# Optimization experiments

Hardware: AMD Instinct MI355X
Metric: run time of the kernel (lower is better)

The kernel has to match this reference:

```python
import jax, jax.numpy as jnp
import numpy as np
from jax import lax

B, IC, OC, H, W_DIM, K = 8, 64, 64, 256, 512, 3
BLUR_1D = [1.0, 3.0, 3.0, 1.0]
FACTOR = 2
GAIN = 1.0


def _blur_kernel():
    # setup_resample_kernel: outer product of 1D kernel, normalized to sum 1
    k = np.asarray(BLUR_1D, dtype=np.float32)
    k = np.outer(k, k)
    k = k / np.sum(k)
    return k  # [4,4]


def setup_inputs() -> dict:
    key = jax.random.key(0)
    ks = jax.random.split(key, 5)
    x = jax.random.normal(ks[0], (B, IC, H, H), dtype=jnp.float32)
    w = jax.random.normal(ks[1], (B, W_DIM), dtype=jnp.float32)
    # init_std = 1.0 for both weights since lrmul = 1.0
    w_conv = jax.random.normal(ks[2], (K, K, IC, OC), dtype=jnp.float32)
    w_dense = jax.random.normal(ks[3], (W_DIM, IC), dtype=jnp.float32)
    b_mod = jnp.zeros((IC,), dtype=jnp.float32)
    return {"x": x, "w": w, "w_conv": w_conv, "w_dense": w_dense, "b_mod": b_mod}


def reference(x, w, w_conv, w_dense, b_mod):
    k = w_conv.shape[0]
    ic, oc = w_conv.shape[2], w_conv.shape[3]

    # runtime coefs (equalized lr): he_std = gain / sqrt(fan_in), lrmul = 1
    coef_conv = 1.0 / np.sqrt(k * k * ic)
    coef_dense = 1.0 / np.sqrt(w.shape[1])

    # style = Dense(w) + bias (linear act, gain 1) + 1.0   -> [B, IC]
    style = w @ (coef_dense * w_dense) + b_mod + 1.0

    # modulate: [B,k,k,IC,OC]
    wmod = (coef_conv * w_conv)[None] * style[:, None, None, :, None]
    # demodulate over (kh, kw, ic)
    d = lax.rsqrt(jnp.sum(jnp.square(wmod), axis=(1, 2, 3)) + 1e-8)  # [B,OC]
    wmod = wmod * d[:, None, None, None, :]

    # per-sample grouped transposed conv (upsample x2) == lhs-dilated cross-corr
    # with the unflipped modulated weight, padding k-1 on each side.
    w_oihw = jnp.transpose(wmod, (0, 4, 3, 1, 2))  # [B,OC,IC,k,k]

    def up_conv(xb, wb):
        return lax.conv_general_dilated(
            xb[None], wb, window_strides=(1, 1),
            padding=[(k - 1, k - 1), (k - 1, k - 1)],
            lhs_dilation=(FACTOR, FACTOR),
            dimension_numbers=("NCHW", "OIHW", "NCHW"))[0]

    y = jax.vmap(up_conv)(x, w_oihw)  # [B,OC,(H-1)*2+k,(W-1)*2+k] = [B,OC,513,513]

    # upfirdn blur: kernel scaled by gain * factor**2, pad0 = pad1 = 1,
    # true convolution (kernel flipped in reference) applied depthwise.
    kb = jnp.asarray(_blur_kernel() * (GAIN * FACTOR ** 2))  # [4,4]
    fw = kb[::-1, ::-1][None, None]  # [1,1,4,4]
    b_, c_, s1, s2 = y.shape
    y = lax.conv_general_dilated(
        y.reshape(b_ * c_, 1, s1, s2), fw, window_strides=(1, 1),
        padding=[(1, 1), (1, 1)],
        dimension_numbers=("NCHW", "OIHW", "NCHW"))
    # output spatial: s1 + 2 - 4 + 1 = 2H
    return y.reshape(b_, c_, y.shape[2], y.shape[3])
```

## Files before the change

kernel.cpp:

```cpp
#include <hip/hip_runtime.h>

#define NB 8
#define IC 64
#define OC 64
#define HH 256
#define WD 512
#define PP 258

typedef __bf16 bf16x8 __attribute__((ext_vector_type(8)));
typedef float f32x16 __attribute__((ext_vector_type(16)));
typedef float f32x2 __attribute__((ext_vector_type(2)));

__device__ inline void compute_E(const float* __restrict__ w_conv, float stv,
                                 int oc, float E[6][6]) {
  const float coef_conv = 1.0f / 24.0f;
  const float s = stv * coef_conv;
  const int ic = threadIdx.x & 63;

  float wm[3][3];
  float ssq = 0.f;
  #pragma unroll
  for (int kh = 0; kh < 3; ++kh)
    #pragma unroll
    for (int kw = 0; kw < 3; ++kw) {
      float v = w_conv[((kh * 3 + kw) * IC + ic) * OC + oc] * s;
      wm[kh][kw] = v;
      ssq += v * v;
    }
  #pragma unroll
  for (int off = 32; off > 0; off >>= 1) ssq += __shfl_xor(ssq, off);
  const float d = rsqrtf(ssq + 1e-8f);
  #pragma unroll
  for (int kh = 0; kh < 3; ++kh)
    #pragma unroll
    for (int kw = 0; kw < 3; ++kw) wm[kh][kw] *= d;

  const float g[4] = {0.25f, 0.75f, 0.75f, 0.25f};
  #pragma unroll
  for (int a = 0; a < 6; ++a)
    #pragma unroll
    for (int c = 0; c < 6; ++c) {
      float acc = 0.f;
      #pragma unroll
      for (int dh = 0; dh < 3; ++dh) {
        int u = a - dh;
        if (u < 0 || u > 3) continue;
        #pragma unroll
        for (int dw = 0; dw < 3; ++dw) {
          int v = c - dw;
          if (v < 0 || v > 3) continue;
          acc = fmaf(wm[dh][dw], g[u] * g[v], acc);
        }
      }
      E[a][c] = acc;
    }
}

__device__ inline float style_of(const float* __restrict__ w,
                                 const float* __restrict__ w_dense,
                                 const float* __restrict__ b_mod, int b,
                                 int ic) {
  const float coef_dense = 0.044194173824159216f;
  const float* wr = w + b * WD;
  float acc = 0.f;
  for (int k = 0; k < WD; ++k) acc = fmaf(wr[k], w_dense[k * IC + ic], acc);
  return acc * coef_dense + b_mod[ic] + 1.0f;
}

__global__ __launch_bounds__(64) void pwfs_kernel(
    const float* __restrict__ w, const float* __restrict__ w_dense,
    const float* __restrict__ b_mod, const float* __restrict__ w_conv,
    __bf16* __restrict__ PWf) {
  const int oc = blockIdx.x;
  const int b = blockIdx.y;
  const int ic = threadIdx.x;

  float stv = style_of(w, w_dense, b_mod, b, ic);
  float E[6][6];
  compute_E(w_conv, stv, oc, E);

  const int ks = ic >> 4;
  const int h = (ic >> 3) & 1;
  const int e = ic & 7;
  const int lane = (oc & 31) + 32 * h;
  const int ocg = oc >> 5;

  #pragma unroll
  for (int pp = 0; pp < 2; ++pp)
    #pragma unroll
    for (int pq = 0; pq < 2; ++pq) {
      const int ph = pp * 2 + pq;
      #pragma unroll
      for (int j = 0; j < 3; ++j)
        #pragma unroll
        for (int l = 0; l < 3; ++l) {
          const int tap = j * 3 + l;
          float val = E[2 * j + 1 - pp][2 * l + 1 - pq];
          size_t off =
              ((size_t)(((((b * 4 + ph) * 9 + tap) * 2 + ocg) * 4 + ks)) * 64 +
               lane) * 8 + e;
          PWf[off] = (__bf16)val;
        }
    }
}

#define XS 268
__global__ __launch_bounds__(256) void xtp_kernel(const float* __restrict__ x,
                                                  __bf16* __restrict__ xTg) {
  __shared__ unsigned short buf[64 * XS];
  const int tid = threadIdx.x;
  const int m = blockIdx.x;
  const int b = blockIdx.y;

  if (m == 256) {
    uint4 z = make_uint4(0, 0, 0, 0);
    for (int i = tid; i < 8224; i += 256) {
      int pix = i >> 3;
      int sub = i & 7;
      int pr, pc;
      if (pix < 258) {
        pr = 0; pc = pix;
      } else if (pix < 516) {
        pr = 257; pc = pix - 258;
      } else {
        int rem = pix - 516;
        pr = 1 + (rem >> 1);
        pc = (rem & 1) ? 257 : 0;
      }
      *(uint4*)(xTg + ((size_t)(b * PP + pr) * PP + pc) * 64 + sub * 8) = z;
    }
    return;
  }

  const int ln = tid & 63, grp = tid >> 6;
  #pragma unroll
  for (int p = 0; p < 16; ++p) {
    const int ic = p * 4 + grp;
    float4 v = *(const float4*)(x + ((size_t)(b * 64 + ic) * 256 + m) * 256 +
                                ln * 4);
    ushort4 u4;
    u4.x = __builtin_bit_cast(unsigned short, (__bf16)v.x);
    u4.y = __builtin_bit_cast(unsigned short, (__bf16)v.y);
    u4.z = __builtin_bit_cast(unsigned short, (__bf16)v.z);
    u4.w = __builtin_bit_cast(unsigned short, (__bf16)v.w);
    *(ushort4*)&buf[ic * XS + ln * 4] = u4;
  }
  __syncthreads();
  #pragma unroll
  for (int it = 0; it < 8; ++it) {
    int pix = it * 32 + (tid >> 3);
    int g = tid & 7;
    bf16x8 o;
    #pragma unroll
    for (int e = 0; e < 8; ++e)
      o[e] = __builtin_bit_cast(__bf16, buf[(g * 8 + e) * XS + pix]);
    *(bf16x8*)(xTg + ((size_t)(b * PP + m + 1) * PP + (pix + 1)) * 64 +
               g * 8) = o;
  }
}

#define CMT 4
#define XR 6
#define XC 34

__device__ __forceinline__ void loadA(const bf16x8* __restrict__ Av, int phb,
                                      int ocg, int ks, int l, int lane,
                                      bf16x8 A[3][2]) {
  #pragma unroll
  for (int j = 0; j < 3; ++j) {
    const int tap = j * 3 + l;
    #pragma unroll
    for (int pq = 0; pq < 2; ++pq)
      A[j][pq] =
          Av[(size_t)((((phb + pq) * 9 + tap) * 2 + ocg) * 4 + ks) * 64 + lane];
  }
}

#define GLD_LDS(src, dst)                                                \
  __builtin_amdgcn_global_load_lds(                                      \
      (const __attribute__((address_space(1))) void*)(src),              \
      (__attribute__((address_space(3))) void*)(dst), 16, 0, 0)

__device__ __forceinline__ void stage6(const __bf16* __restrict__ xTg, int b,
                                       int m0, int n0, __bf16* xsbuf, int wv,
                                       int lane) {
  if (wv < XR) {
    const int row = wv;
    const size_t srow = (size_t)(b * PP + m0 + row) * PP;
    __bf16* ldsrow = xsbuf + row * (XC * 64);
    #pragma unroll
    for (int q = 0; q < 4; ++q) {
      int pix = q * 8 + (lane >> 3);
      int g = (lane & 7) ^ (pix & 7);
      const __bf16* src = xTg + (srow + (n0 + pix)) * 64 + g * 8;
      GLD_LDS(src, ldsrow + q * 512);
    }
    if (lane < 16) {
      int pix = 32 + (lane >> 3);
      int g = (lane & 7) ^ (pix & 7);
      const __bf16* src = xTg + (srow + (n0 + pix)) * 64 + g * 8;
      GLD_LDS(src, ldsrow + 2048);
    }
  }
}

__global__ __launch_bounds__(512, 4) void conv32d_kernel(
    const __bf16* __restrict__ xTg, const __bf16* __restrict__ PWf,
    float* __restrict__ out) {
  __shared__ __bf16 xs[2][XR * XC * 64];

  const int tid = threadIdx.x;
  const int lane = tid & 63;
  const int wv = tid >> 6;
  const int pp = wv & 1;
  const int og = (wv >> 1) & 1;
  const int rh = wv >> 2;

  const int raw = blockIdx.x;
  const int bid = (raw & 7) * 64 + (raw >> 3);
  const int mtile = bid & 63;
  const int b = bid >> 6;
  const int m0 = mtile * CMT;

  const int ln31 = lane & 31;
  const int lh = lane >> 5;
  const bf16x8* Av = (const bf16x8*)PWf;
  const int phb = b * 4 + pp * 2;

  stage6(xTg, b, m0, 0, &xs[0][0], wv, lane);
  asm volatile("s_waitcnt vmcnt(0)" ::: "memory");
  __builtin_amdgcn_s_barrier();

  #pragma unroll 1
  for (int t = 0; t < 8; ++t) {
    const int n0 = t * 32;
    if (t < 7) stage6(xTg, b, m0, n0 + 32, &xs[(t + 1) & 1][0], wv, lane);

    const __bf16* xb = &xs[t & 1][0];

    f32x16 acc[2][2];
    #pragma unroll
    for (int mw = 0; mw < 2; ++mw)
      #pragma unroll
      for (int pq = 0; pq < 2; ++pq)
        #pragma unroll
        for (int e = 0; e < 16; ++e) acc[mw][pq][e] = 0.f;

    int ks = 0, l = 0;
    #pragma unroll 1
    for (int it = 0; it < 12; ++it) {
      bf16x8 Ac[3][2];
      loadA(Av, phb, og, ks, l, lane, Ac);

      bf16x8 Bf[4];
      const int col_t = ln31 + l;
      const int gneed = ks * 2 + lh;
      #pragma unroll
      for (int r = 0; r < 4; ++r) {
        const int lds_row = 2 * rh + r;
        Bf[r] = *(const bf16x8*)(xb + ((lds_row * XC + col_t) * 8 +
                                       (gneed ^ (col_t & 7))) * 8);
      }

      __builtin_amdgcn_s_setprio(1);
      #pragma unroll
      for (int r = 0; r < 4; ++r) {
        #pragma unroll
        for (int j = 0; j < 3; ++j) {
          const int mw = r - j;
          if (mw == 0 || mw == 1) {
            acc[mw][0] = __builtin_amdgcn_mfma_f32_32x32x16_bf16(
                Ac[j][0], Bf[r], acc[mw][0], 0, 0, 0);
            acc[mw][1] = __builtin_amdgcn_mfma_f32_32x32x16_bf16(
                Ac[j][1], Bf[r], acc[mw][1], 0, 0, 0);
          }
        }
      }
      __builtin_amdgcn_s_setprio(0);

      l = (l == 2) ? 0 : l + 1;
      ks = (l == 0) ? (ks + 1) & 3 : ks;
    }

    asm volatile("s_waitcnt vmcnt(0)" ::: "memory");

    #pragma unroll
    for (int mw = 0; mw < 2; ++mw) {
      const int p = 2 * (m0 + 2 * rh + mw) + pp;
      #pragma unroll
      for (int rr = 0; rr < 16; ++rr) {
        const int oc_loc = (rr & 3) + 8 * (rr >> 2) + 4 * lh;
        const int oc = og * 32 + oc_loc;
        size_t off =
            ((size_t)(b * 64 + oc) * 512 + p) * 512 + 2 * n0 + 2 * ln31;
        f32x2 v2;
        v2[0] = acc[mw][0][rr];
        v2[1] = acc[mw][1][rr];
        __builtin_nontemporal_store(v2, (f32x2*)(out + off));
      }
    }

    if (t < 7) __builtin_amdgcn_s_barrier();
  }
}

__global__ __launch_bounds__(64) void pw_kernel(
    const float* __restrict__ w, const float* __restrict__ w_dense,
    const float* __restrict__ b_mod, const float* __restrict__ w_conv,
    float* __restrict__ PW) {
  const int oc = blockIdx.x;
  const int b = blockIdx.y;
  const int ic = threadIdx.x;
  float stv = style_of(w, w_dense, b_mod, b, ic);
  float E[6][6];
  compute_E(w_conv, stv, oc, E);
  #pragma unroll
  for (int pp = 0; pp < 2; ++pp)
    #pragma unroll
    for (int pq = 0; pq < 2; ++pq)
      #pragma unroll
      for (int j = 0; j < 3; ++j)
        #pragma unroll
        for (int l = 0; l < 3; ++l)
          PW[(((size_t)((b * 4 + pp * 2 + pq) * OC + oc) * IC + ic) * 9) +
             j * 3 + l] = E[2 * j + 1 - pp][2 * l + 1 - pq];
}

#define MT 16
#define NT 64
#define ICC 8
#define XROWS 18
#define XCOLS 66
#define XSTRIDE 68

__global__ __launch_bounds__(256) void conv_kernel(
    const float* __restrict__ x, const float* __restrict__ PW,
    float* __restrict__ out) {
  __shared__ float lds_x[ICC][XROWS][XSTRIDE];
  __shared__ float lds_w[4][ICC][9][4];

  const int tid = threadIdx.x;
  const int tn = tid & 15;
  const int tm = tid >> 4;
  const int bx = blockIdx.x;
  const int ntile = bx & 3;
  const int mtile = bx >> 2;
  const int ocg = blockIdx.y;
  const int b = blockIdx.z;
  const int m0 = mtile * MT;
  const int n0 = ntile * NT;

  float acc[4][4][4];
  #pragma unroll
  for (int o = 0; o < 4; ++o)
    #pragma unroll
    for (int ph = 0; ph < 4; ++ph)
      #pragma unroll
      for (int s = 0; s < 4; ++s) acc[o][ph][s] = 0.f;

  for (int ic0 = 0; ic0 < IC; ic0 += ICC) {
    __syncthreads();
    for (int ici = 0; ici < ICC; ++ici) {
      const float* xsrc = x + (size_t)(b * IC + ic0 + ici) * HH * HH;
      for (int rc = tid; rc < XROWS * XCOLS; rc += 256) {
        int r = rc / XCOLS;
        int c = rc - r * XCOLS;
        int gr = m0 - 1 + r;
        int gc = n0 - 1 + c;
        float v = 0.f;
        if ((unsigned)gr < HH && (unsigned)gc < HH) v = xsrc[gr * HH + gc];
        lds_x[ici][r][c] = v;
      }
    }
    for (int idx = tid; idx < 4 * ICC * 9 * 4; idx += 256) {
      int o = idx / (ICC * 9 * 4);
      int rem = idx - o * (ICC * 9 * 4);
      int ici = rem / 36;
      int r2 = rem - ici * 36;
      int t = r2 >> 2;
      int ph = r2 & 3;
      lds_w[o][ici][t][ph] =
          PW[(((size_t)((b * 4 + ph) * OC + (ocg * 4 + o)) * IC +
               (ic0 + ici)) * 9) + t];
    }
    __syncthreads();
    for (int ici = 0; ici < ICC; ++ici) {
      #pragma unroll
      for (int j = 0; j < 3; ++j) {
        const float* xr = &lds_x[ici][tm + j][tn * 4];
        float4 a4 = *(const float4*)xr;
        float2 a2 = *(const float2*)(xr + 4);
        float xv[6] = {a4.x, a4.y, a4.z, a4.w, a2.x, a2.y};
        #pragma unroll
        for (int l = 0; l < 3; ++l) {
          #pragma unroll
          for (int o = 0; o < 4; ++o) {
            float4 wv = *(const float4*)&lds_w[o][ici][j * 3 + l][0];
            #pragma unroll
            for (int s = 0; s < 4; ++s) {
              acc[o][0][s] = fmaf(wv.x, xv[l + s], acc[o][0][s]);
              acc[o][1][s] = fmaf(wv.y, xv[l + s], acc[o][1][s]);
              acc[o][2][s] = fmaf(wv.z, xv[l + s], acc[o][2][s]);
              acc[o][3][s] = fmaf(wv.w, xv[l + s], acc[o][3][s]);
            }
          }
        }
      }
    }
  }

  #pragma unroll
  for (int o = 0; o < 4; ++o) {
    #pragma unroll
    for (int pp = 0; pp < 2; ++pp) {
      const int p = 2 * (m0 + tm) + pp;
      float* dst = out +
          (((size_t)(b * OC + ocg * 4 + o) * 512 + p) * 512) + 2 * n0 + 8 * tn;
      float4 v0 = make_float4(acc[o][pp * 2 + 0][0], acc[o][pp * 2 + 1][0],
                              acc[o][pp * 2 + 0][1], acc[o][pp * 2 + 1][1]);
      float4 v1 = make_float4(acc[o][pp * 2 + 0][2], acc[o][pp * 2 + 1][2],
                              acc[o][pp * 2 + 0][3], acc[o][pp * 2 + 1][3]);
      *(float4*)dst = v0;
      *(float4*)(dst + 4) = v1;
    }
  }
}

extern "C" void kernel_launch(void* const* d_in, const int* in_sizes, int n_in,
                              void* d_out, int out_size, void* d_ws,
                              size_t ws_size, hipStream_t stream) {
  const float* x = (const float*)d_in[0];
  const float* w = (const float*)d_in[1];
  const float* w_conv = (const float*)d_in[2];
  const float* w_dense = (const float*)d_in[3];
  const float* b_mod = (const float*)d_in[4];
  float* out = (float*)d_out;

  const size_t PWF_BYTES = (size_t)8 * 4 * 9 * 2 * 4 * 64 * 8 * 2;
  const size_t XTG_BYTES = (size_t)8 * PP * PP * 64 * 2;
  const size_t NEED_NEW = PWF_BYTES + XTG_BYTES;

  if (ws_size >= NEED_NEW) {
    __bf16* PWf = (__bf16*)d_ws;
    __bf16* xTg = (__bf16*)((char*)d_ws + PWF_BYTES);
    pwfs_kernel<<<dim3(OC, NB), 64, 0, stream>>>(w, w_dense, b_mod, w_conv,
                                                 PWf);
    xtp_kernel<<<dim3(257, NB), 256, 0, stream>>>(x, xTg);
    conv32d_kernel<<<dim3(512), 512, 0, stream>>>(xTg, PWf, out);
  } else {
    float* PW = (float*)d_ws;
    pw_kernel<<<dim3(OC, NB), 64, 0, stream>>>(w, w_dense, b_mod, w_conv, PW);
    conv_kernel<<<dim3(64, 16, NB), 256, 0, stream>>>(x, PW, out);
  }
}
```

Baseline: 260.8 us.

## Use 1024-thread blocks with 8-row tiles and per-wave phase split

The conv kernel now uses 1024-thread blocks covering 8 input rows (10 staged LDS rows) instead of 4, with each wave owning one output phase column and four row-accumulators rather than two phases by two rows. The aim is better reuse of the staged x tile and of the weight fragments, at the cost of scalar 4-byte stores in place of paired 8-byte stores. The final vmcnt(0) wait moves to a partial wait between store batches. The grid halves to 256 blocks, which risks leaving CUs underused on a 256-CU part, and the stores become less coalesced.

```diff
diff --git a/kernel.cpp b/kernel.cpp
--- a/kernel.cpp
+++ b/kernel.cpp
@@ -159,31 +159,18 @@
   }
 }
 
-#define CMT 4
-#define XR 6
+#define CMT 8
+#define XR 10
 #define XC 34
-
-__device__ __forceinline__ void loadA(const bf16x8* __restrict__ Av, int phb,
-                                      int ocg, int ks, int l, int lane,
-                                      bf16x8 A[3][2]) {
-  #pragma unroll
-  for (int j = 0; j < 3; ++j) {
-    const int tap = j * 3 + l;
-    #pragma unroll
-    for (int pq = 0; pq < 2; ++pq)
-      A[j][pq] =
-          Av[(size_t)((((phb + pq) * 9 + tap) * 2 + ocg) * 4 + ks) * 64 + lane];
-  }
-}
 
 #define GLD_LDS(src, dst)                                                \
   __builtin_amdgcn_global_load_lds(                                      \
       (const __attribute__((address_space(1))) void*)(src),              \
       (__attribute__((address_space(3))) void*)(dst), 16, 0, 0)
 
-__device__ __forceinline__ void stage6(const __bf16* __restrict__ xTg, int b,
-                                       int m0, int n0, __bf16* xsbuf, int wv,
-                                       int lane) {
+__device__ __forceinline__ void stage10(const __bf16* __restrict__ xTg, int b,
+                                        int m0, int n0, __bf16* xsbuf, int wv,
+                                        int lane) {
   if (wv < XR) {
     const int row = wv;
     const size_t srow = (size_t)(b * PP + m0 + row) * PP;
@@ -204,7 +191,7 @@
   }
 }
 
-__global__ __launch_bounds__(512, 4) void conv32d_kernel(
+__global__ __launch_bounds__(1024, 4) void conv32q_kernel(
     const __bf16* __restrict__ xTg, const __bf16* __restrict__ PWf,
     float* __restrict__ out) {
   __shared__ __bf16 xs[2][XR * XC * 64];
@@ -212,67 +199,66 @@
   const int tid = threadIdx.x;
   const int lane = tid & 63;
   const int wv = tid >> 6;
-  const int pp = wv & 1;
-  const int og = (wv >> 1) & 1;
-  const int rh = wv >> 2;
+  const int pq = wv & 1;
+  const int pp = (wv >> 1) & 1;
+  const int og = (wv >> 2) & 1;
+  const int rh = wv >> 3;
 
   const int raw = blockIdx.x;
-  const int bid = (raw & 7) * 64 + (raw >> 3);
-  const int mtile = bid & 63;
-  const int b = bid >> 6;
+  const int bid = (raw & 7) * 32 + (raw >> 3);
+  const int mtile = bid & 31;
+  const int b = bid >> 5;
   const int m0 = mtile * CMT;
 
   const int ln31 = lane & 31;
   const int lh = lane >> 5;
-  const bf16x8* Av = (const bf16x8*)PWf;
-  const int phb = b * 4 + pp * 2;
-
-  stage6(xTg, b, m0, 0, &xs[0][0], wv, lane);
+  const int ph = b * 4 + pp * 2 + pq;
+  const bf16x8* Awave =
+      (const bf16x8*)PWf + ((size_t)ph * 72 + og * 4) * 64 + lane;
+
+  stage10(xTg, b, m0, 0, &xs[0][0], wv, lane);
   asm volatile("s_waitcnt vmcnt(0)" ::: "memory");
   __builtin_amdgcn_s_barrier();
 
   #pragma unroll 1
   for (int t = 0; t < 8; ++t) {
     const int n0 = t * 32;
-    if (t < 7) stage6(xTg, b, m0, n0 + 32, &xs[(t + 1) & 1][0], wv, lane);
+    if (t < 7) stage10(xTg, b, m0, n0 + 32, &xs[(t + 1) & 1][0], wv, lane);
 
     const __bf16* xb = &xs[t & 1][0];
 
-    f32x16 acc[2][2];
-    #pragma unroll
-    for (int mw = 0; mw < 2; ++mw)
-      #pragma unroll
-      for (int pq = 0; pq < 2; ++pq)
-        #pragma unroll
-        for (int e = 0; e < 16; ++e) acc[mw][pq][e] = 0.f;
+    f32x16 acc[4];
+    #pragma unroll
+    for (int mw = 0; mw < 4; ++mw)
+      #pragma unroll
+      for (int e = 0; e < 16; ++e) acc[mw][e] = 0.f;
 
     int ks = 0, l = 0;
     #pragma unroll 1
     for (int it = 0; it < 12; ++it) {
-      bf16x8 Ac[3][2];
-      loadA(Av, phb, og, ks, l, lane, Ac);
-
-      bf16x8 Bf[4];
+      bf16x8 A[3];
+      #pragma unroll
+      for (int j = 0; j < 3; ++j) A[j] = Awave[((j * 3 + l) * 8 + ks) * 64];
+
+      bf16x8 Bf[6];
       const int col_t = ln31 + l;
       const int gneed = ks * 2 + lh;
       #pragma unroll
-      for (int r = 0; r < 4; ++r) {
-        const int lds_row = 2 * rh + r;
+      for (int r = 0; r < 6; ++r) {
+        const int lds_row = 4 * rh + r;
         Bf[r] = *(const bf16x8*)(xb + ((lds_row * XC + col_t) * 8 +
                                        (gneed ^ (col_t & 7))) * 8);
       }
 
       __builtin_amdgcn_s_setprio(1);
       #pragma unroll
-      for (int r = 0; r < 4; ++r) {
+      for (int r = 0; r < 6; ++r) {
         #pragma unroll
         for (int j = 0; j < 3; ++j) {
           const int mw = r - j;
-          if (mw == 0 || mw == 1) {
-            acc[mw][0] = __builtin_amdgcn_mfma_f32_32x32x16_bf16(
-                Ac[j][0], Bf[r], acc[mw][0], 0, 0, 0);
-            acc[mw][1] = __builtin_amdgcn_mfma_f32_32x32x16_bf16(
-                Ac[j][1], Bf[r], acc[mw][1], 0, 0, 0);
+          if (mw >= 0 && mw < 4) {
+            acc[mw] = __builtin_amdgcn_mfma_f32_32x32x16_bf16(A[j], Bf[r],
+                                                              acc[mw], 0, 0, 0);
           }
         }
       }
@@ -282,21 +268,29 @@
       ks = (l == 0) ? (ks + 1) & 3 : ks;
     }
 
-    asm volatile("s_waitcnt vmcnt(0)" ::: "memory");
-
     #pragma unroll
     for (int mw = 0; mw < 2; ++mw) {
-      const int p = 2 * (m0 + 2 * rh + mw) + pp;
+      const int p = 2 * (m0 + 4 * rh + mw) + pp;
       #pragma unroll
       for (int rr = 0; rr < 16; ++rr) {
         const int oc_loc = (rr & 3) + 8 * (rr >> 2) + 4 * lh;
         const int oc = og * 32 + oc_loc;
-        size_t off =
-            ((size_t)(b * 64 + oc) * 512 + p) * 512 + 2 * n0 + 2 * ln31;
-        f32x2 v2;
-        v2[0] = acc[mw][0][rr];
-        v2[1] = acc[mw][1][rr];
-        __builtin_nontemporal_store(v2, (f32x2*)(out + off));
+        size_t off = ((size_t)(b * 64 + oc) * 512 + p) * 512 +
+                     2 * (n0 + ln31) + pq;
+        __builtin_nontemporal_store(acc[mw][rr], out + off);
+      }
+    }
+    asm volatile("s_waitcnt vmcnt(32)" ::: "memory");
+    #pragma unroll
+    for (int mw = 2; mw < 4; ++mw) {
+      const int p = 2 * (m0 + 4 * rh + mw) + pp;
+      #pragma unroll
+      for (int rr = 0; rr < 16; ++rr) {
+        const int oc_loc = (rr & 3) + 8 * (rr >> 2) + 4 * lh;
+        const int oc = og * 32 + oc_loc;
+        size_t off = ((size_t)(b * 64 + oc) * 512 + p) * 512 +
+                     2 * (n0 + ln31) + pq;
+        __builtin_nontemporal_store(acc[mw][rr], out + off);
       }
     }
 
@@ -446,7 +440,7 @@
     pwfs_kernel<<<dim3(OC, NB), 64, 0, stream>>>(w, w_dense, b_mod, w_conv,
                                                  PWf);
     xtp_kernel<<<dim3(257, NB), 256, 0, stream>>>(x, xTg);
-    conv32d_kernel<<<dim3(512), 512, 0, stream>>>(xTg, PWf, out);
+    conv32q_kernel<<<dim3(256), 1024, 0, stream>>>(xTg, PWf, out);
   } else {
     float* PW = (float*)d_ws;
     pw_kernel<<<dim3(OC, NB), 64, 0, stream>>>(w, w_dense, b_mod, w_conv, PW);
```

Result: slower. 426.7 us (+63.6%).
